# Kernel optimization log

Measured on AMD Instinct MI355X. Metric: run time of the kernel, lower is better.

The kernel has to match this reference:

```python
import jax, jax.numpy as jnp
import numpy as np

WIN = (8, 8)
DIM = 256
HEADS = 8
B = 2048
NW = 64


def _make_buffers(win):
    wh, ww = win
    # relative_position_bias_table: (1, 2wh-1, 2ww-1, 2)
    rh = np.arange(-(wh - 1), wh, dtype=np.float32)
    rw = np.arange(-(ww - 1), ww, dtype=np.float32)
    gh, gw = np.meshgrid(rh, rw, indexing='ij')
    tbl = np.stack([gh, gw], axis=-1)[None]  # (1, 2wh-1, 2ww-1, 2)
    tbl[..., 0] /= (wh - 1)
    tbl[..., 1] /= (ww - 1)
    tbl *= 3.2
    tbl = np.sign(tbl) * (1.0 - np.exp(-np.abs(tbl)))
    # relative_position_index: (n, n)
    ch, cw = np.meshgrid(np.arange(wh), np.arange(ww), indexing='ij')
    cf = np.stack([ch.reshape(-1), cw.reshape(-1)])  # (2, n)
    rel = cf[:, :, None] - cf[:, None, :]            # (2, n, n)
    rel = rel.transpose(1, 2, 0).astype(np.int64)
    rel[..., 0] += wh - 1
    rel[..., 1] += ww - 1
    rel[..., 0] *= 2 * ww - 1
    rpi = rel.sum(-1).astype(np.int32)
    return jnp.asarray(tbl, dtype=jnp.float32), jnp.asarray(rpi)


def setup_inputs() -> dict:
    key = jax.random.key(0)
    ks = jax.random.split(key, 12)
    c2 = DIM // 2
    n = WIN[0] * WIN[1]
    s = 0.02
    inp = {
        'x': jax.random.normal(ks[0], (B, n, DIM), dtype=jnp.float32),
        'mask': jax.random.normal(ks[1], (NW, n, n), dtype=jnp.float32),
        'qw': jax.random.normal(ks[2], (2, c2, c2), dtype=jnp.float32) * s,
        'qb': jnp.zeros((2, c2), dtype=jnp.float32),
        'kw': jax.random.normal(ks[3], (2, c2, c2), dtype=jnp.float32) * s,
        'kb': jnp.zeros((2, c2), dtype=jnp.float32),
        'vw': jax.random.normal(ks[4], (2, c2, c2), dtype=jnp.float32) * s,
        'vb': jnp.zeros((2, c2), dtype=jnp.float32),
        'pw': jax.random.normal(ks[5], (2, c2, c2), dtype=jnp.float32) * s,
        'pb': jnp.zeros((2, c2), dtype=jnp.float32),
        'mlp_w1': jax.random.normal(ks[6], (2, 128), dtype=jnp.float32) * s,
        'mlp_b1': jnp.zeros((128,), dtype=jnp.float32),
        'mlp_w2': jax.random.normal(ks[7], (128, HEADS), dtype=jnp.float32) * s,
        'logit_scale': jnp.full((HEADS, 1, 1), np.log(10.0), dtype=jnp.float32),
    }
    tbl, rpi = _make_buffers(WIN)
    inp['rpb_table'] = tbl
    inp['rpi'] = rpi
    return inp


def _l2norm(v, eps=1e-12):
    nrm = jnp.sqrt(jnp.sum(v * v, axis=-1, keepdims=True))
    return v / jnp.maximum(nrm, eps)


def _forward(x, mask, qw, qb, kw, kb, vw, vb, pw, pb,
             mlp_w1, mlp_b1, mlp_w2, logit_scale, rpb_table, rpi):
    b, n, c = x.shape
    h = logit_scale.shape[0]
    c2 = c // 2
    hd = c // h
    xb = x.reshape(b, n, 2, c2)  # branch split on channel halves

    def dual(w, bias):  # residual dual-branch linear: xb + Linear(xb)
        return xb + jnp.einsum('bnsc,scd->bnsd', xb, w) + bias

    # (b, n, 2, c2) -> (b, n, c) -> (b, h, n, hd)
    q = dual(qw, qb).reshape(b, n, h, hd).transpose(0, 2, 1, 3)
    k = dual(kw, kb).reshape(b, n, h, hd).transpose(0, 2, 1, 3)
    v = dual(vw, vb).reshape(b, n, h, hd).transpose(0, 2, 1, 3)

    attn = jnp.einsum('bhnd,bhmd->bhnm', _l2norm(q), _l2norm(k))
    scale = jnp.exp(jnp.minimum(logit_scale, jnp.log(jnp.float32(100.0))))  # (h,1,1)
    attn = attn * scale[None]

    # CPB-MLP relative position bias
    hid = jax.nn.relu(rpb_table @ mlp_w1 + mlp_b1)         # (1, 2wh-1, 2ww-1, 128)
    tbl = (hid @ mlp_w2).reshape(-1, h)                    # ((2wh-1)(2ww-1), h)
    bias = tbl[rpi.reshape(-1)].reshape(n, n, h).transpose(2, 0, 1)
    attn = attn + 16.0 * jax.nn.sigmoid(bias)[None]

    if mask is not None:
        nw = mask.shape[0]
        attn = attn.reshape(b // nw, nw, h, n, n) + mask[None, :, None]
        attn = attn.reshape(b, h, n, n)

    attn = jax.nn.softmax(attn, axis=-1)
    out = jnp.einsum('bhnm,bhmd->bhnd', attn, v).transpose(0, 2, 1, 3).reshape(b, n, c)

    ob = out.reshape(b, n, 2, c2)
    y = jnp.einsum('bnsc,scd->bnsd', ob, pw) + pb
    return y.reshape(b, n, c)


def reference(x, mask, qw, qb, kw, kb, vw, vb, pw, pb,
              mlp_w1, mlp_b1, mlp_w2, logit_scale, rpb_table, rpi):
    return _forward(x, mask, qw, qb, kw, kb, vw, vb, pw, pb,
                    mlp_w1, mlp_b1, mlp_w2, logit_scale, rpb_table, rpi)
```

## Files before the change

kernel.cpp:

```cpp
#include <hip/hip_runtime.h>
#include <stdint.h>

#define B_    2048
#define N_    64
#define C_    256
#define C2_   128
#define H_    8
#define NW_   64
#define NPOS  225

typedef __attribute__((ext_vector_type(8))) short short8;
typedef __attribute__((ext_vector_type(4))) float float4v;

__device__ float g_scale[H_];
__device__ float g_t8[NPOS][H_];
__device__ __align__(16) float g_sb[NW_ * H_ * N_ * N_];
__device__ unsigned short g_wt[4][2][C2_][C2_];

__device__ __forceinline__ float b2f(unsigned short u) {
  return __uint_as_float(((unsigned int)u) << 16);
}
__device__ __forceinline__ unsigned short f2b(float f) {
  unsigned int u = __float_as_uint(f);
  u += 0x7fffu + ((u >> 16) & 1u);
  return (unsigned short)(u >> 16);
}

__global__ __launch_bounds__(256) void k_prep1(
    const float* __restrict__ tbl, const float* __restrict__ w1,
    const float* __restrict__ b1, const float* __restrict__ w2,
    const float* __restrict__ ls) {
  __shared__ float sw1[256], sb1[128], sw2[1024];
  const int t = threadIdx.x;
  sw1[t] = w1[t];
  if (t < 128) sb1[t] = b1[t];
#pragma unroll
  for (int it = 0; it < 4; ++it) sw2[it * 256 + t] = w2[it * 256 + t];
  __syncthreads();
  if (t < NPOS) {
    float a0 = tbl[2 * t], a1 = tbl[2 * t + 1];
    float acc[H_];
#pragma unroll
    for (int h = 0; h < H_; ++h) acc[h] = 0.f;
    for (int j = 0; j < 128; ++j) {
      float hid = fmaxf(a0 * sw1[j] + a1 * sw1[128 + j] + sb1[j], 0.f);
#pragma unroll
      for (int h = 0; h < H_; ++h) acc[h] += hid * sw2[j * H_ + h];
    }
#pragma unroll
    for (int h = 0; h < H_; ++h) g_t8[t][h] = acc[h];
  }
  if (t < H_) g_scale[t] = __expf(fminf(ls[t], 4.6051702f));
}

__global__ __launch_bounds__(256) void k_prep2(
    const float* __restrict__ mask, const int* __restrict__ rpi) {
  const int base = blockIdx.x * 1024;
#pragma unroll
  for (int it = 0; it < 4; ++it) {
    int idx = base + it * 256 + threadIdx.x;
    int i  = idx & 63;
    int j  = (idx >> 6) & 63;
    int h  = (idx >> 12) & 7;
    int wd = idx >> 15;
    float v = g_t8[rpi[i * 64 + j]][h];
    g_sb[idx] = 16.f / (1.f + __expf(-v)) + mask[wd * 4096 + i * 64 + j];
  }
}

__global__ __launch_bounds__(256) void k_prepw(
    const float* __restrict__ qw, const float* __restrict__ kw,
    const float* __restrict__ vw, const float* __restrict__ pw) {
  __shared__ unsigned short lt[128 * 132];
  const int t = threadIdx.x;
  const int p = blockIdx.x >> 1, s = blockIdx.x & 1;
  const float* src = (p == 0 ? qw : p == 1 ? kw : p == 2 ? vw : pw) + s * (C2_ * C2_);
#pragma unroll
  for (int it = 0; it < 64; ++it) {
    int e = it * 256 + t;
    int c = e >> 7, d = e & 127;
    lt[d * 132 + c] = f2b(src[e]);
  }
  __syncthreads();
#pragma unroll
  for (int it = 0; it < 64; ++it) {
    int e = it * 256 + t;
    int d = e >> 7, c = e & 127;
    g_wt[p][s][d][c] = lt[d * 132 + c];
  }
}

__global__ __launch_bounds__(512) void k_main(
    const float* __restrict__ x, float* __restrict__ out,
    const float* __restrict__ qb, const float* __restrict__ kb,
    const float* __restrict__ vb, const float* __restrict__ pb) {
  __shared__ __align__(16) unsigned short xs[N_ * 264];
  __shared__ __align__(16) unsigned short qs[N_ * 264];
  __shared__ __align__(16) unsigned short ks[N_ * 264];
  __shared__ __align__(16) unsigned short vt[C_ * 72];
  __shared__ __align__(16) unsigned short pl[8 * 16 * 72];

  const int t    = threadIdx.x;
  const int lane = t & 63;
  const int w    = __builtin_amdgcn_readfirstlane(t >> 6);
  const int b    = blockIdx.x;
  const int l15  = lane & 15;
  const int qd   = lane >> 4;

  {
    const float4* xg = (const float4*)(x + (size_t)b * (N_ * C_));
#pragma unroll
    for (int it = 0; it < 8; ++it) {
      int e = t + 512 * it;
      int row = e >> 6, c4 = (e & 63) << 2;
      float4 v = xg[e];
      uint2 pk;
      pk.x = ((unsigned)f2b(v.y) << 16) | f2b(v.x);
      pk.y = ((unsigned)f2b(v.w) << 16) | f2b(v.z);
      *(uint2*)&xs[row * 264 + c4] = pk;
    }
  }
  __syncthreads();

  const int s1 = w >> 2;
  const int jl = 32 * (w & 3);
  const float scl = g_scale[s1 * 4 + (w & 3)];
  for (int pj = 0; pj < 3; ++pj) {
    const float* bi = pj == 0 ? qb : (pj == 1 ? kb : vb);
    float4v acc[4][2];
    {
      float b0 = bi[s1 * C2_ + jl + l15], b1 = bi[s1 * C2_ + jl + 16 + l15];
#pragma unroll
      for (int mt = 0; mt < 4; ++mt) {
        acc[mt][0] = float4v{b0, b0, b0, b0};
        acc[mt][1] = float4v{b1, b1, b1, b1};
      }
    }
    const unsigned short* wt = &g_wt[pj][s1][0][0];
#pragma unroll
    for (int kc = 0; kc < 4; ++kc) {
      int ko = kc * 32 + qd * 8;
      short8 a[4], bf[2];
#pragma unroll
      for (int mt = 0; mt < 4; ++mt)
        a[mt] = *(const short8*)&xs[(mt * 16 + l15) * 264 + s1 * 128 + ko];
      bf[0] = *(const short8*)&wt[(jl + l15) * C2_ + ko];
      bf[1] = *(const short8*)&wt[(jl + 16 + l15) * C2_ + ko];
#pragma unroll
      for (int mt = 0; mt < 4; ++mt)
#pragma unroll
        for (int nt = 0; nt < 2; ++nt)
          acc[mt][nt] = __builtin_amdgcn_mfma_f32_16x16x32_bf16(
              a[mt], bf[nt], acc[mt][nt], 0, 0, 0);
    }
    unsigned short* dst = pj == 0 ? qs : ks;
#pragma unroll
    for (int mt = 0; mt < 4; ++mt) {
      int row0 = mt * 16 + qd * 4;
      float vv[2][4];
#pragma unroll
      for (int nt = 0; nt < 2; ++nt)
#pragma unroll
        for (int r = 0; r < 4; ++r)
          vv[nt][r] = acc[mt][nt][r] +
                      b2f(xs[(row0 + r) * 264 + s1 * 128 + jl + nt * 16 + l15]);
      if (pj < 2) {
        float ss[4];
#pragma unroll
        for (int r = 0; r < 4; ++r) ss[r] = vv[0][r] * vv[0][r] + vv[1][r] * vv[1][r];
#pragma unroll
        for (int m = 1; m < 16; m <<= 1)
#pragma unroll
          for (int r = 0; r < 4; ++r) ss[r] += __shfl_xor(ss[r], m, 64);
#pragma unroll
        for (int r = 0; r < 4; ++r) {
          float rn = 1.0f / fmaxf(sqrtf(ss[r]), 1e-12f);
          if (pj == 0) rn *= scl;
          vv[0][r] *= rn;
          vv[1][r] *= rn;
        }
#pragma unroll
        for (int nt = 0; nt < 2; ++nt)
#pragma unroll
          for (int r = 0; r < 4; ++r)
            dst[(row0 + r) * 264 + s1 * 128 + jl + nt * 16 + l15] = f2b(vv[nt][r]);
      } else {
#pragma unroll
        for (int nt = 0; nt < 2; ++nt) {
          int chan = s1 * 128 + jl + nt * 16 + l15;
          uint2 pk;
          pk.x = ((unsigned)f2b(vv[nt][1]) << 16) | f2b(vv[nt][0]);
          pk.y = ((unsigned)f2b(vv[nt][3]) << 16) | f2b(vv[nt][2]);
          *(uint2*)&vt[chan * 72 + row0] = pk;
        }
      }
    }
  }
  __syncthreads();

  const int wm = w & 3, wg = w >> 2;
  unsigned short* plw = pl + w * (16 * 72);
  const float* sbb = g_sb + (size_t)(b & 63) * (H_ * N_ * N_);
#pragma unroll
  for (int hh = 0; hh < 4; ++hh) {
    const int h = 4 * wg + hh;
    const float* sbh = sbb + h * 4096;
    short8 aq = *(const short8*)&qs[(16 * wm + l15) * 264 + h * 32 + qd * 8];
    float4v sacc[4];
#pragma unroll
    for (int nt = 0; nt < 4; ++nt) {
      float4 cv = *(const float4*)&sbh[(nt * 16 + l15) * 64 + 16 * wm + qd * 4];
      float4v c = {cv.x, cv.y, cv.z, cv.w};
      short8 bk = *(const short8*)&ks[(nt * 16 + l15) * 264 + h * 32 + qd * 8];
      sacc[nt] = __builtin_amdgcn_mfma_f32_16x16x32_bf16(aq, bk, c, 0, 0, 0);
    }
    float e[4][4], rs[4];
#pragma unroll
    for (int r = 0; r < 4; ++r) rs[r] = 0.f;
#pragma unroll
    for (int nt = 0; nt < 4; ++nt)
#pragma unroll
      for (int r = 0; r < 4; ++r) {
        e[nt][r] = __expf(sacc[nt][r]);
        rs[r] += e[nt][r];
      }
#pragma unroll
    for (int m = 1; m < 16; m <<= 1)
#pragma unroll
      for (int r = 0; r < 4; ++r) rs[r] += __shfl_xor(rs[r], m, 64);
    float rr[4];
#pragma unroll
    for (int r = 0; r < 4; ++r) rr[r] = 1.0f / rs[r];
#pragma unroll
    for (int nt = 0; nt < 4; ++nt)
#pragma unroll
      for (int r = 0; r < 4; ++r)
        plw[(qd * 4 + r) * 72 + nt * 16 + l15] = f2b(e[nt][r] * rr[r]);
    float4v oacc[2];
    oacc[0] = float4v{0, 0, 0, 0};
    oacc[1] = float4v{0, 0, 0, 0};
#pragma unroll
    for (int kc = 0; kc < 2; ++kc) {
      short8 ap = *(const short8*)&plw[l15 * 72 + kc * 32 + qd * 8];
#pragma unroll
      for (int nt2 = 0; nt2 < 2; ++nt2) {
        short8 bv = *(const short8*)&vt[(h * 32 + nt2 * 16 + l15) * 72 + kc * 32 + qd * 8];
        oacc[nt2] = __builtin_amdgcn_mfma_f32_16x16x32_bf16(ap, bv, oacc[nt2], 0, 0, 0);
      }
    }
#pragma unroll
    for (int nt2 = 0; nt2 < 2; ++nt2)
#pragma unroll
      for (int r = 0; r < 4; ++r)
        xs[(16 * wm + qd * 4 + r) * 264 + h * 32 + nt2 * 16 + l15] = f2b(oacc[nt2][r]);
  }
  __syncthreads();

  {
    float4v acc[4][2];
    float b0 = pb[s1 * C2_ + jl + l15], b1 = pb[s1 * C2_ + jl + 16 + l15];
#pragma unroll
    for (int mt = 0; mt < 4; ++mt) {
      acc[mt][0] = float4v{b0, b0, b0, b0};
      acc[mt][1] = float4v{b1, b1, b1, b1};
    }
    const unsigned short* wt = &g_wt[3][s1][0][0];
#pragma unroll
    for (int kc = 0; kc < 4; ++kc) {
      int ko = kc * 32 + qd * 8;
      short8 a[4], bf[2];
#pragma unroll
      for (int mt = 0; mt < 4; ++mt)
        a[mt] = *(const short8*)&xs[(mt * 16 + l15) * 264 + s1 * 128 + ko];
      bf[0] = *(const short8*)&wt[(jl + l15) * C2_ + ko];
      bf[1] = *(const short8*)&wt[(jl + 16 + l15) * C2_ + ko];
#pragma unroll
      for (int mt = 0; mt < 4; ++mt)
#pragma unroll
        for (int nt = 0; nt < 2; ++nt)
          acc[mt][nt] = __builtin_amdgcn_mfma_f32_16x16x32_bf16(
              a[mt], bf[nt], acc[mt][nt], 0, 0, 0);
    }
#pragma unroll
    for (int mt = 0; mt < 4; ++mt)
#pragma unroll
      for (int nt = 0; nt < 2; ++nt)
#pragma unroll
        for (int r = 0; r < 4; ++r)
          out[((size_t)b * N_ + mt * 16 + qd * 4 + r) * C_ +
              s1 * 128 + jl + nt * 16 + l15] = acc[mt][nt][r];
  }
}

extern "C" void kernel_launch(void* const* d_in, const int* in_sizes, int n_in,
                              void* d_out, int out_size, void* d_ws, size_t ws_size,
                              hipStream_t stream) {
  const float* x    = (const float*)d_in[0];
  const float* mask = (const float*)d_in[1];
  const float* qw   = (const float*)d_in[2];
  const float* qb   = (const float*)d_in[3];
  const float* kw   = (const float*)d_in[4];
  const float* kb   = (const float*)d_in[5];
  const float* vw   = (const float*)d_in[6];
  const float* vb   = (const float*)d_in[7];
  const float* pw   = (const float*)d_in[8];
  const float* pb   = (const float*)d_in[9];
  const float* w1   = (const float*)d_in[10];
  const float* b1   = (const float*)d_in[11];
  const float* w2   = (const float*)d_in[12];
  const float* ls   = (const float*)d_in[13];
  const float* tbl  = (const float*)d_in[14];
  const int*   rpi  = (const int*)d_in[15];
  float* out = (float*)d_out;

  k_prep1<<<1, 256, 0, stream>>>(tbl, w1, b1, w2, ls);
  k_prep2<<<2048, 256, 0, stream>>>(mask, rpi);
  k_prepw<<<8, 256, 0, stream>>>(qw, kw, vw, pw);
  k_main<<<B_, 512, 0, stream>>>(x, out, qb, kb, vb, pb);
}
```

Before: 413.3 us.

## Double warps per block and keep softmax probabilities in registers via transposed scores

Raises the block size from 512 to 1024 threads and splits each projection GEMM's rows across wave pairs, so each wave handles half the M tiles and two heads instead of four. The score MFMA now takes K as the A operand and Q as the B operand, with the bias table stored transposed in k_prep2 to match. Softmax row sums then need only two cross-lane shuffles. The normalized probabilities are packed to bf16 and redistributed with lane shuffles into the A-operand layout, removing the per-wave LDS staging buffer and its writes and reads. Risks include heavier register pressure under launch_bounds(1024,4) and extra shuffle instructions.

```diff
diff --git a/kernel.cpp b/kernel.cpp
--- a/kernel.cpp
+++ b/kernel.cpp
@@ -11,6 +11,8 @@
 
 typedef __attribute__((ext_vector_type(8))) short short8;
 typedef __attribute__((ext_vector_type(4))) float float4v;
+
+union U8 { unsigned u[4]; short8 s; };
 
 __device__ float g_scale[H_];
 __device__ float g_t8[NPOS][H_];
@@ -59,8 +61,8 @@
 #pragma unroll
   for (int it = 0; it < 4; ++it) {
     int idx = base + it * 256 + threadIdx.x;
-    int i  = idx & 63;
-    int j  = (idx >> 6) & 63;
+    int j  = idx & 63;
+    int i  = (idx >> 6) & 63;
     int h  = (idx >> 12) & 7;
     int wd = idx >> 15;
     float v = g_t8[rpi[i * 64 + j]][h];
@@ -90,7 +92,7 @@
   }
 }
 
-__global__ __launch_bounds__(512) void k_main(
+__global__ __launch_bounds__(1024, 4) void k_main(
     const float* __restrict__ x, float* __restrict__ out,
     const float* __restrict__ qb, const float* __restrict__ kb,
     const float* __restrict__ vb, const float* __restrict__ pb) {
@@ -98,7 +100,6 @@
   __shared__ __align__(16) unsigned short qs[N_ * 264];
   __shared__ __align__(16) unsigned short ks[N_ * 264];
   __shared__ __align__(16) unsigned short vt[C_ * 72];
-  __shared__ __align__(16) unsigned short pl[8 * 16 * 72];
 
   const int t    = threadIdx.x;
   const int lane = t & 63;
@@ -110,8 +111,8 @@
   {
     const float4* xg = (const float4*)(x + (size_t)b * (N_ * C_));
 #pragma unroll
-    for (int it = 0; it < 8; ++it) {
-      int e = t + 512 * it;
+    for (int it = 0; it < 4; ++it) {
+      int e = t + 1024 * it;
       int row = e >> 6, c4 = (e & 63) << 2;
       float4 v = xg[e];
       uint2 pk;
@@ -122,16 +123,18 @@
   }
   __syncthreads();
 
-  const int s1 = w >> 2;
-  const int jl = 32 * (w & 3);
-  const float scl = g_scale[s1 * 4 + (w & 3)];
+  const int s1 = w >> 3;
+  const int jls = (w >> 1) & 3;
+  const int jl = 32 * jls;
+  const int mh = w & 1;
+  const float scl = g_scale[s1 * 4 + jls];
   for (int pj = 0; pj < 3; ++pj) {
     const float* bi = pj == 0 ? qb : (pj == 1 ? kb : vb);
-    float4v acc[4][2];
+    float4v acc[2][2];
     {
       float b0 = bi[s1 * C2_ + jl + l15], b1 = bi[s1 * C2_ + jl + 16 + l15];
 #pragma unroll
-      for (int mt = 0; mt < 4; ++mt) {
+      for (int mt = 0; mt < 2; ++mt) {
         acc[mt][0] = float4v{b0, b0, b0, b0};
         acc[mt][1] = float4v{b1, b1, b1, b1};
       }
@@ -140,14 +143,14 @@
 #pragma unroll
     for (int kc = 0; kc < 4; ++kc) {
       int ko = kc * 32 + qd * 8;
-      short8 a[4], bf[2];
-#pragma unroll
-      for (int mt = 0; mt < 4; ++mt)
-        a[mt] = *(const short8*)&xs[(mt * 16 + l15) * 264 + s1 * 128 + ko];
+      short8 a[2], bf[2];
+#pragma unroll
+      for (int mt = 0; mt < 2; ++mt)
+        a[mt] = *(const short8*)&xs[(32 * mh + mt * 16 + l15) * 264 + s1 * 128 + ko];
       bf[0] = *(const short8*)&wt[(jl + l15) * C2_ + ko];
       bf[1] = *(const short8*)&wt[(jl + 16 + l15) * C2_ + ko];
 #pragma unroll
-      for (int mt = 0; mt < 4; ++mt)
+      for (int mt = 0; mt < 2; ++mt)
 #pragma unroll
         for (int nt = 0; nt < 2; ++nt)
           acc[mt][nt] = __builtin_amdgcn_mfma_f32_16x16x32_bf16(
@@ -155,8 +158,8 @@
     }
     unsigned short* dst = pj == 0 ? qs : ks;
 #pragma unroll
-    for (int mt = 0; mt < 4; ++mt) {
-      int row0 = mt * 16 + qd * 4;
+    for (int mt = 0; mt < 2; ++mt) {
+      int row0 = 32 * mh + mt * 16 + qd * 4;
       float vv[2][4];
 #pragma unroll
       for (int nt = 0; nt < 2; ++nt)
@@ -199,49 +202,60 @@
   __syncthreads();
 
   const int wm = w & 3, wg = w >> 2;
-  unsigned short* plw = pl + w * (16 * 72);
   const float* sbb = g_sb + (size_t)(b & 63) * (H_ * N_ * N_);
-#pragma unroll
-  for (int hh = 0; hh < 4; ++hh) {
-    const int h = 4 * wg + hh;
+  const int hi_sel = lane & 32;
+  const int src0 = l15 | ((((qd << 1) + 0) & 3) << 4);
+  const int src1 = l15 | ((((qd << 1) + 1) & 3) << 4);
+#pragma unroll
+  for (int hh = 0; hh < 2; ++hh) {
+    const int h = 2 * wg + hh;
     const float* sbh = sbb + h * 4096;
-    short8 aq = *(const short8*)&qs[(16 * wm + l15) * 264 + h * 32 + qd * 8];
+    short8 bq = *(const short8*)&qs[(16 * wm + l15) * 264 + h * 32 + qd * 8];
     float4v sacc[4];
 #pragma unroll
     for (int nt = 0; nt < 4; ++nt) {
-      float4 cv = *(const float4*)&sbh[(nt * 16 + l15) * 64 + 16 * wm + qd * 4];
+      float4 cv = *(const float4*)&sbh[(16 * wm + l15) * 64 + nt * 16 + qd * 4];
       float4v c = {cv.x, cv.y, cv.z, cv.w};
-      short8 bk = *(const short8*)&ks[(nt * 16 + l15) * 264 + h * 32 + qd * 8];
-      sacc[nt] = __builtin_amdgcn_mfma_f32_16x16x32_bf16(aq, bk, c, 0, 0, 0);
-    }
-    float e[4][4], rs[4];
-#pragma unroll
-    for (int r = 0; r < 4; ++r) rs[r] = 0.f;
+      short8 ak = *(const short8*)&ks[(nt * 16 + l15) * 264 + h * 32 + qd * 8];
+      sacc[nt] = __builtin_amdgcn_mfma_f32_16x16x32_bf16(ak, bq, c, 0, 0, 0);
+    }
+    float e[4][4];
+    float s = 0.f;
 #pragma unroll
     for (int nt = 0; nt < 4; ++nt)
 #pragma unroll
       for (int r = 0; r < 4; ++r) {
         e[nt][r] = __expf(sacc[nt][r]);
-        rs[r] += e[nt][r];
+        s += e[nt][r];
       }
-#pragma unroll
-    for (int m = 1; m < 16; m <<= 1)
-#pragma unroll
-      for (int r = 0; r < 4; ++r) rs[r] += __shfl_xor(rs[r], m, 64);
-    float rr[4];
-#pragma unroll
-    for (int r = 0; r < 4; ++r) rr[r] = 1.0f / rs[r];
+    s += __shfl_xor(s, 16, 64);
+    s += __shfl_xor(s, 32, 64);
+    float rr = 1.0f / s;
+    unsigned pk[4][2];
 #pragma unroll
     for (int nt = 0; nt < 4; ++nt)
 #pragma unroll
-      for (int r = 0; r < 4; ++r)
-        plw[(qd * 4 + r) * 72 + nt * 16 + l15] = f2b(e[nt][r] * rr[r]);
+      for (int rp = 0; rp < 2; ++rp)
+        pk[nt][rp] = ((unsigned)f2b(e[nt][2 * rp + 1] * rr) << 16) |
+                     f2b(e[nt][2 * rp] * rr);
+    U8 au[2];
+#pragma unroll
+    for (int j2 = 0; j2 < 4; ++j2) {
+      int src = (j2 >> 1) ? src1 : src0;
+      int rp = j2 & 1;
+      int r0 = __shfl((int)pk[0][rp], src, 64);
+      int r1 = __shfl((int)pk[1][rp], src, 64);
+      int r2 = __shfl((int)pk[2][rp], src, 64);
+      int r3 = __shfl((int)pk[3][rp], src, 64);
+      au[0].u[j2] = hi_sel ? (unsigned)r1 : (unsigned)r0;
+      au[1].u[j2] = hi_sel ? (unsigned)r3 : (unsigned)r2;
+    }
     float4v oacc[2];
     oacc[0] = float4v{0, 0, 0, 0};
     oacc[1] = float4v{0, 0, 0, 0};
 #pragma unroll
     for (int kc = 0; kc < 2; ++kc) {
-      short8 ap = *(const short8*)&plw[l15 * 72 + kc * 32 + qd * 8];
+      short8 ap = au[kc].s;
 #pragma unroll
       for (int nt2 = 0; nt2 < 2; ++nt2) {
         short8 bv = *(const short8*)&vt[(h * 32 + nt2 * 16 + l15) * 72 + kc * 32 + qd * 8];
@@ -257,10 +271,10 @@
   __syncthreads();
 
   {
-    float4v acc[4][2];
+    float4v acc[2][2];
     float b0 = pb[s1 * C2_ + jl + l15], b1 = pb[s1 * C2_ + jl + 16 + l15];
 #pragma unroll
-    for (int mt = 0; mt < 4; ++mt) {
+    for (int mt = 0; mt < 2; ++mt) {
       acc[mt][0] = float4v{b0, b0, b0, b0};
       acc[mt][1] = float4v{b1, b1, b1, b1};
     }
@@ -268,26 +282,26 @@
 #pragma unroll
     for (int kc = 0; kc < 4; ++kc) {
       int ko = kc * 32 + qd * 8;
-      short8 a[4], bf[2];
-#pragma unroll
-      for (int mt = 0; mt < 4; ++mt)
-        a[mt] = *(const short8*)&xs[(mt * 16 + l15) * 264 + s1 * 128 + ko];
+      short8 a[2], bf[2];
+#pragma unroll
+      for (int mt = 0; mt < 2; ++mt)
+        a[mt] = *(const short8*)&xs[(32 * mh + mt * 16 + l15) * 264 + s1 * 128 + ko];
       bf[0] = *(const short8*)&wt[(jl + l15) * C2_ + ko];
       bf[1] = *(const short8*)&wt[(jl + 16 + l15) * C2_ + ko];
 #pragma unroll
-      for (int mt = 0; mt < 4; ++mt)
+      for (int mt = 0; mt < 2; ++mt)
 #pragma unroll
         for (int nt = 0; nt < 2; ++nt)
           acc[mt][nt] = __builtin_amdgcn_mfma_f32_16x16x32_bf16(
               a[mt], bf[nt], acc[mt][nt], 0, 0, 0);
     }
 #pragma unroll
-    for (int mt = 0; mt < 4; ++mt)
+    for (int mt = 0; mt < 2; ++mt)
 #pragma unroll
       for (int nt = 0; nt < 2; ++nt)
 #pragma unroll
         for (int r = 0; r < 4; ++r)
-          out[((size_t)b * N_ + mt * 16 + qd * 4 + r) * C_ +
+          out[((size_t)b * N_ + 32 * mh + mt * 16 + qd * 4 + r) * C_ +
               s1 * 128 + jl + nt * 16 + l15] = acc[mt][nt][r];
   }
 }
@@ -316,5 +330,5 @@
   k_prep1<<<1, 256, 0, stream>>>(tbl, w1, b1, w2, ls);
   k_prep2<<<2048, 256, 0, stream>>>(mask, rpi);
   k_prepw<<<8, 256, 0, stream>>>(qw, kw, vw, pw);
-  k_main<<<B_, 512, 0, stream>>>(x, out, qb, kb, vb, pb);
-}
+  k_main<<<B_, 1024, 0, stream>>>(x, out, qb, kb, vb, pb);
+}
```

New measurement: 421.0 us. About the same (+1.9%).
